# Kernel optimization log

Measured on AMD Instinct MI355X. Metric: run time of the kernel, lower is better.

## Reference

```python
import jax, jax.numpy as jnp
import numpy as np

N_HEADS = 2


def _ln(x, g, b, eps=1e-5):
    m = x.mean(-1, keepdims=True)
    v = ((x - m) ** 2).mean(-1, keepdims=True)
    return (x - m) * jax.lax.rsqrt(v + eps) * g + b


def _mha(x, in_w, in_b, out_w, out_b):
    # standard multi-head self-attention (relative/rotary branch is inert: query_pos=None)
    B, S, d = x.shape
    hd = d // N_HEADS
    qkv = x @ in_w.T + in_b
    q, k, v = jnp.split(qkv, 3, axis=-1)
    q = q.reshape(B, S, N_HEADS, hd)
    k = k.reshape(B, S, N_HEADS, hd)
    v = v.reshape(B, S, N_HEADS, hd)
    scores = jnp.einsum('bqhd,bkhd->bhqk', q, k) / jnp.sqrt(jnp.asarray(hd, x.dtype))
    attn = jax.nn.softmax(scores, axis=-1)
    o = jnp.einsum('bhqk,bkhd->bqhd', attn, v).reshape(B, S, d)
    return o @ out_w.T + out_b


def _forward(x, w1, b1, attn_in_w, attn_in_b, attn_out_w, attn_out_b, ln1_g, ln1_b,
             ffw_w1, ffw_b1, ffw_w2, ffw_b2, ln2_g, ln2_b,
             in_proj_w, conv_w, conv_b, x_proj_w, dt_proj_w, dt_proj_b, A_log, D, out_proj_w,
             w2a, b2a, w2b, b2b, w3a, b3a, w3b, b3b):
    # mlp1: (B,S,1) -> (B,S,d)
    h = x @ w1.T + b1
    # FFWRelativeSelfAttentionModule: 2 layers of post-norm MHA + FFW, take last output
    for i in range(2):
        a = _mha(h, attn_in_w[i], attn_in_b[i], attn_out_w[i], attn_out_b[i])
        h = _ln(h + a, ln1_g[i], ln1_b[i])
        f = jax.nn.relu(h @ ffw_w1[i].T + ffw_b1[i]) @ ffw_w2[i].T + ffw_b2[i]
        h = _ln(h + f, ln2_g[i], ln2_b[i])
    # Mamba block
    xz = h @ in_proj_w.T                       # (B,S,2*di)
    xm, z = jnp.split(xz, 2, axis=-1)          # (B,S,di) each
    S_len = xm.shape[1]
    dcv = conv_w.shape[1]
    xp = jnp.pad(xm, ((0, 0), (dcv - 1, 0), (0, 0)))   # causal depthwise conv1d
    xc = conv_b + sum(conv_w[:, k] * xp[:, k:k + S_len, :] for k in range(dcv))
    xc = jax.nn.silu(xc)
    xdb = xc @ x_proj_w.T                      # (B,S,dt_rank+2*N)
    dt_r = dt_proj_w.shape[1]
    N = A_log.shape[1]
    dti = xdb[..., :dt_r]
    Bm = xdb[..., dt_r:dt_r + N]
    Cm = xdb[..., dt_r + N:]
    dt = jax.nn.softplus(dti @ dt_proj_w.T + dt_proj_b)   # (B,S,di)
    A = -jnp.exp(A_log)                                    # (di,N)

    def step(hst, inp):
        dt_t, B_t, C_t, x_t = inp              # (B,di),(B,N),(B,N),(B,di)
        hst = hst * jnp.exp(dt_t[..., None] * A) + dt_t[..., None] * B_t[:, None, :] * x_t[..., None]
        y = jnp.einsum('bdn,bn->bd', hst, C_t)
        return hst, y

    h0 = jnp.zeros((xc.shape[0], A.shape[0], N), xc.dtype)
    xs = (jnp.swapaxes(dt, 0, 1), jnp.swapaxes(Bm, 0, 1),
          jnp.swapaxes(Cm, 0, 1), jnp.swapaxes(xc, 0, 1))
    _, ys = jax.lax.scan(step, h0, xs)
    y = jnp.swapaxes(ys, 0, 1) + D * xc
    y = y * jax.nn.silu(z)
    h = y @ out_proj_w.T                       # (B,S,d)
    # mlp2 (two stacked Linears, no activation) -> (B,S,1)
    o = (h @ w2a.T + b2a) @ w2b.T + b2b
    o = o.reshape(o.shape[0], -1)              # (B,9)
    # mlp3
    o = jax.nn.relu(o @ w3a.T + b3a) @ w3b.T + b3b
    return o


def setup_inputs() -> dict:
    key = jax.random.key(0)
    ks = jax.random.split(key, 16)
    d, N, dcv, di, dtr, B, S = 256, 16, 4, 512, 16, 4096, 9
    rn = lambda k, shp, s=0.02: jax.random.normal(k, shp, jnp.float32) * s
    return {
        'x': jax.random.normal(ks[0], (B, S, 1), jnp.float32),
        'w1': rn(ks[1], (d, 1), 0.5), 'b1': jnp.zeros((d,)),
        'attn_in_w': rn(ks[2], (2, 3 * d, d)), 'attn_in_b': jnp.zeros((2, 3 * d)),
        'attn_out_w': rn(ks[3], (2, d, d)), 'attn_out_b': jnp.zeros((2, d)),
        'ln1_g': jnp.ones((2, d)), 'ln1_b': jnp.zeros((2, d)),
        'ffw_w1': rn(ks[4], (2, d, d)), 'ffw_b1': jnp.zeros((2, d)),
        'ffw_w2': rn(ks[5], (2, d, d)), 'ffw_b2': jnp.zeros((2, d)),
        'ln2_g': jnp.ones((2, d)), 'ln2_b': jnp.zeros((2, d)),
        'in_proj_w': rn(ks[6], (2 * di, d)),
        'conv_w': rn(ks[7], (di, dcv), 0.2), 'conv_b': jnp.zeros((di,)),
        'x_proj_w': rn(ks[8], (dtr + 2 * N, di)),
        'dt_proj_w': rn(ks[9], (di, dtr), 0.1), 'dt_proj_b': jnp.full((di,), -4.0),
        'A_log': jnp.log(jnp.broadcast_to(jnp.arange(1, N + 1, dtype=jnp.float32), (di, N))),
        'D': jnp.ones((di,)),
        'out_proj_w': rn(ks[10], (d, di)),
        'w2a': rn(ks[11], (32, d)), 'b2a': jnp.zeros((32,)),
        'w2b': rn(ks[12], (1, 32)), 'b2b': jnp.zeros((1,)),
        'w3a': rn(ks[13], (9, 9), 0.3), 'b3a': jnp.zeros((9,)),
        'w3b': rn(ks[14], (1, 9), 0.3), 'b3b': jnp.zeros((1,)),
    }


def reference(x, w1, b1, attn_in_w, attn_in_b, attn_out_w, attn_out_b, ln1_g, ln1_b,
              ffw_w1, ffw_b1, ffw_w2, ffw_b2, ln2_g, ln2_b,
              in_proj_w, conv_w, conv_b, x_proj_w, dt_proj_w, dt_proj_b, A_log, D, out_proj_w,
              w2a, b2a, w2b, b2b, w3a, b3a, w3b, b3b):
    return _forward(x, w1, b1, attn_in_w, attn_in_b, attn_out_w, attn_out_b, ln1_g, ln1_b,
                    ffw_w1, ffw_b1, ffw_w2, ffw_b2, ln2_g, ln2_b,
                    in_proj_w, conv_w, conv_b, x_proj_w, dt_proj_w, dt_proj_b, A_log, D, out_proj_w,
                    w2a, b2a, w2b, b2b, w3a, b3a, w3b, b3b)
```

## Files before the change

kernel.cpp:

```cpp
#include <hip/hip_runtime.h>
#include <hip/hip_bf16.h>
#include <math.h>


#define BATCH 4096

typedef __attribute__((ext_vector_type(8))) short short8;
typedef __attribute__((ext_vector_type(4))) float f32x4;
typedef __attribute__((ext_vector_type(4))) unsigned short u16x4;
typedef unsigned short ushort;

#define GLD16(gp, lp) __builtin_amdgcn_global_load_lds( \
    (const __attribute__((address_space(1))) unsigned int*)(gp), \
    (__attribute__((address_space(3))) unsigned int*)(lp), 16, 0, 0)

__device__ __forceinline__ ushort f2bf(float f) {
    unsigned u = __float_as_uint(f);
    u += 0x7fffu + ((u >> 16) & 1u);
    return (ushort)(u >> 16);
}
__device__ __forceinline__ float bf2f(ushort u) {
    return __uint_as_float(((unsigned)u) << 16);
}

__global__ __launch_bounds__(256) void convw_kernel(
    const float* __restrict__ s0, const float* __restrict__ s1,
    const float* __restrict__ s2, const float* __restrict__ s3,
    const float* __restrict__ s4, const float* __restrict__ s5,
    ushort* __restrict__ dst)
{
    int i = blockIdx.x * 256 + threadIdx.x;
    float v;
    if      (i < 393216)  v = s0[i];
    else if (i < 524288)  v = s1[i - 393216];
    else if (i < 655360)  v = s2[i - 524288];
    else if (i < 786432)  v = s3[i - 655360];
    else if (i < 1048576) v = s4[i - 786432];
    else                  v = s5[i - 1048576];
    dst[i] = f2bf(v);
}

__global__ __launch_bounds__(512) void headw_kernel(
    const float* __restrict__ out_proj_w,
    const float* __restrict__ w2a,
    const float* __restrict__ b2a,
    const float* __restrict__ w2b,
    const float* __restrict__ b2b,
    float* __restrict__ wcb)
{
    __shared__ float vc[256];
    const int t = threadIdx.x;
    if (t < 256) {
        float a = 0.f;
        #pragma unroll
        for (int j = 0; j < 32; ++j) a = fmaf(w2b[j], w2a[j * 256 + t], a);
        vc[t] = a;
    }
    __syncthreads();
    float a = 0.f;
    for (int c = 0; c < 256; ++c) a = fmaf(vc[c], out_proj_w[c * 512 + t], a);
    wcb[t] = a;
    if (t == 0) {
        float bc = b2b[0];
        #pragma unroll
        for (int j = 0; j < 32; ++j) bc = fmaf(w2b[j], b2a[j], bc);
        wcb[512] = bc;
    }
}

__global__ __launch_bounds__(256) void embed_kernel(
    const float* __restrict__ x, const float* __restrict__ w1,
    const float* __restrict__ b1, float* __restrict__ h,
    ushort* __restrict__ hbf, int r0, int nr)
{
    int i = blockIdx.x * 256 + threadIdx.x;
    if (i >= nr * 256) return;
    int c  = i & 255;
    int row = i >> 8;
    float v = x[r0 + row] * w1[c] + b1[c];
    h[i] = v;
    hbf[i] = f2bf(v);
}

__global__ __launch_bounds__(256) void mgemm_kernel(
    const ushort* __restrict__ A, const ushort* __restrict__ W,
    const float* __restrict__ bias, float* __restrict__ Cf,
    ushort* __restrict__ Cb, const float* __restrict__ yin,
    int M, int N, int K, int lda, int act, int outmode)
{
    __shared__ ushort As[128 * 64];
    __shared__ ushort Bs[128 * 64];

    const int tid  = threadIdx.x;
    const int m0   = blockIdx.x * 128;
    const int n0   = blockIdx.y * 128;
    const int wid  = tid >> 6, lane = tid & 63;
    const int wr   = wid >> 1, wc = wid & 1;
    const int lrow = lane & 15, lk8 = lane >> 4, l7 = lane & 7;
    const int rw   = lane >> 3, sl8 = lane & 7;

    f32x4 acc[4][4];
    #pragma unroll
    for (int i = 0; i < 4; ++i)
        #pragma unroll
        for (int j = 0; j < 4; ++j)
            acc[i][j] = f32x4{0.f, 0.f, 0.f, 0.f};

    for (int k0 = 0; k0 < K; k0 += 64) {
        const int ka = (sl8 ^ rw) * 8;
        #pragma unroll
        for (int p = 0; p < 4; ++p) {
            const int r0 = (p * 4 + wid) * 8;
            const int r  = r0 + rw;
            GLD16(&A[(size_t)(m0 + r) * lda + k0 + ka], &As[r0 * 64]);
            GLD16(&W[(size_t)(n0 + r) * K   + k0 + ka], &Bs[r0 * 64]);
        }
        __syncthreads();

        #pragma unroll
        for (int kh = 0; kh < 2; ++kh) {
            short8 af[4], bf[4];
            #pragma unroll
            for (int i = 0; i < 4; ++i) {
                const int ra = wr * 64 + i * 16 + lrow;
                const int rb = wc * 64 + i * 16 + lrow;
                const int sl = ((kh << 2) | lk8) ^ l7;
                af[i] = *reinterpret_cast<const short8*>(&As[ra * 64 + sl * 8]);
                bf[i] = *reinterpret_cast<const short8*>(&Bs[rb * 64 + sl * 8]);
            }
            #pragma unroll
            for (int i = 0; i < 4; ++i)
                #pragma unroll
                for (int j = 0; j < 4; ++j)
                    acc[i][j] = __builtin_amdgcn_mfma_f32_16x16x32_bf16(
                        af[i], bf[j], acc[i][j], 0, 0, 0);
        }
        __syncthreads();
    }

    const int cb = n0 + wc * 64 + lrow;
    const int rb = m0 + wr * 64 + lk8 * 4;
    float bj[4];
    #pragma unroll
    for (int j = 0; j < 4; ++j) bj[j] = bias ? bias[cb + j * 16] : 0.f;

    #pragma unroll
    for (int i = 0; i < 4; ++i) {
        #pragma unroll
        for (int r = 0; r < 4; ++r) {
            const size_t mrow = (size_t)(rb + i * 16 + r) * N;
            #pragma unroll
            for (int j = 0; j < 4; ++j) {
                float v = acc[i][j][r] + bj[j];
                const size_t idx = mrow + cb + j * 16;
                if (act == 1) v = fmaxf(v, 0.f);
                if (outmode == 0) {
                    Cf[idx] = v;
                } else if (outmode == 1) {
                    Cb[idx] = f2bf(v);
                } else {
                    const float sig = 1.f / (1.f + __expf(-v));
                    Cb[idx] = f2bf(yin[idx] * (v * sig));
                }
            }
        }
    }
}

__global__ __launch_bounds__(256) void sgemm_kernel(
    const float* __restrict__ A, const float* __restrict__ W,
    const float* __restrict__ bias, float* __restrict__ C,
    int M, int N, int K, int lda, int act)
{
    __shared__ float As[16][68];
    __shared__ float Ws[16][68];
    const int tid = threadIdx.x;
    const int m0 = blockIdx.y * 64;
    const int n0 = blockIdx.x * 64;
    const int tm = tid >> 4;
    const int tn = tid & 15;
    const int lrow = tid >> 2;
    const int lk   = (tid & 3) * 4;

    float acc[4][4] = {};

    for (int k0 = 0; k0 < K; k0 += 16) {
        {
            int m = m0 + lrow;
            float4 v = make_float4(0.f, 0.f, 0.f, 0.f);
            if (m < M) v = *reinterpret_cast<const float4*>(&A[(size_t)m * lda + k0 + lk]);
            As[lk + 0][lrow] = v.x; As[lk + 1][lrow] = v.y;
            As[lk + 2][lrow] = v.z; As[lk + 3][lrow] = v.w;
            int n = n0 + lrow;
            float4 w = make_float4(0.f, 0.f, 0.f, 0.f);
            if (n < N) w = *reinterpret_cast<const float4*>(&W[(size_t)n * K + k0 + lk]);
            Ws[lk + 0][lrow] = w.x; Ws[lk + 1][lrow] = w.y;
            Ws[lk + 2][lrow] = w.z; Ws[lk + 3][lrow] = w.w;
        }
        __syncthreads();
        #pragma unroll
        for (int k = 0; k < 16; ++k) {
            float4 av = *reinterpret_cast<const float4*>(&As[k][tm * 4]);
            float4 wv = *reinterpret_cast<const float4*>(&Ws[k][tn * 4]);
            float a[4] = {av.x, av.y, av.z, av.w};
            float w[4] = {wv.x, wv.y, wv.z, wv.w};
            #pragma unroll
            for (int i = 0; i < 4; ++i)
                #pragma unroll
                for (int j = 0; j < 4; ++j)
                    acc[i][j] = fmaf(a[i], w[j], acc[i][j]);
        }
        __syncthreads();
    }

    #pragma unroll
    for (int i = 0; i < 4; ++i) {
        int m = m0 + tm * 4 + i;
        if (m >= M) continue;
        #pragma unroll
        for (int j = 0; j < 4; ++j) {
            int n = n0 + tn * 4 + j;
            if (n >= N) continue;
            float v = acc[i][j];
            if (bias) v += bias[n];
            if (act == 1) v = fmaxf(v, 0.f);
            C[(size_t)m * N + n] = v;
        }
    }
}

__global__ __launch_bounds__(128) void attn_kernel(
    const ushort* __restrict__ qkv, ushort* __restrict__ o, int nb)
{
    __shared__ float q[9][132], kk[9][132], v[9][132];
    __shared__ float sc[9][12];
    const int blk = blockIdx.x;
    if (blk >= nb * 2) return;
    const int b = blk >> 1, head = blk & 1;
    const int t = threadIdx.x;
    const size_t base = (size_t)b * 9 * 768 + (size_t)head * 128;
    #pragma unroll
    for (int s = 0; s < 9; ++s) {
        q[s][t]  = bf2f(qkv[base + s * 768 + t]);
        kk[s][t] = bf2f(qkv[base + s * 768 + 256 + t]);
        v[s][t]  = bf2f(qkv[base + s * 768 + 512 + t]);
    }
    __syncthreads();
    if (t < 81) {
        int qi = t / 9, ki = t % 9;
        float acc = 0.f;
        #pragma unroll 8
        for (int c = 0; c < 128; ++c) acc = fmaf(q[qi][c], kk[ki][c], acc);
        sc[qi][ki] = acc * 0.08838834764831845f;
    }
    __syncthreads();
    if (t < 9) {
        float mx = -1e30f;
        #pragma unroll
        for (int k2 = 0; k2 < 9; ++k2) mx = fmaxf(mx, sc[t][k2]);
        float e[9], sum = 0.f;
        #pragma unroll
        for (int k2 = 0; k2 < 9; ++k2) { e[k2] = __expf(sc[t][k2] - mx); sum += e[k2]; }
        float inv = 1.f / sum;
        #pragma unroll
        for (int k2 = 0; k2 < 9; ++k2) sc[t][k2] = e[k2] * inv;
    }
    __syncthreads();
    #pragma unroll
    for (int qi = 0; qi < 9; ++qi) {
        float acc = 0.f;
        #pragma unroll
        for (int k2 = 0; k2 < 9; ++k2) acc = fmaf(sc[qi][k2], v[k2][t], acc);
        o[(size_t)(b * 9 + qi) * 256 + head * 128 + t] = f2bf(acc);
    }
}

__global__ __launch_bounds__(256) void ln_add_kernel(
    const float* __restrict__ h, const float* __restrict__ a,
    const float* __restrict__ g, const float* __restrict__ bb,
    float* __restrict__ out, ushort* __restrict__ outbf, int nrows)
{
    const int wave = threadIdx.x >> 6;
    const int lane = threadIdx.x & 63;
    const int row = blockIdx.x * 4 + wave;
    if (row >= nrows) return;
    const float4 hv = reinterpret_cast<const float4*>(h + (size_t)row * 256)[lane];
    const float4 av = reinterpret_cast<const float4*>(a + (size_t)row * 256)[lane];
    float x0 = hv.x + av.x, x1 = hv.y + av.y, x2 = hv.z + av.z, x3 = hv.w + av.w;
    float s  = x0 + x1 + x2 + x3;
    float sq = x0 * x0 + x1 * x1 + x2 * x2 + x3 * x3;
    #pragma unroll
    for (int off = 32; off; off >>= 1) {
        s  += __shfl_down(s, off);
        sq += __shfl_down(sq, off);
    }
    s = __shfl(s, 0); sq = __shfl(sq, 0);
    const float mean = s * (1.f / 256.f);
    const float var  = sq * (1.f / 256.f) - mean * mean;
    const float inv  = rsqrtf(var + 1e-5f);
    const float4 gv = reinterpret_cast<const float4*>(g)[lane];
    const float4 bv = reinterpret_cast<const float4*>(bb)[lane];
    float4 ov;
    ov.x = (x0 - mean) * inv * gv.x + bv.x;
    ov.y = (x1 - mean) * inv * gv.y + bv.y;
    ov.z = (x2 - mean) * inv * gv.z + bv.z;
    ov.w = (x3 - mean) * inv * gv.w + bv.w;
    reinterpret_cast<float4*>(out + (size_t)row * 256)[lane] = ov;
    u16x4 bf;
    bf.x = f2bf(ov.x); bf.y = f2bf(ov.y); bf.z = f2bf(ov.z); bf.w = f2bf(ov.w);
    reinterpret_cast<u16x4*>(outbf + (size_t)row * 256)[lane] = bf;
}

__global__ __launch_bounds__(256) void conv_silu2_kernel(
    const float* __restrict__ xm, const float* __restrict__ cw,
    const float* __restrict__ cb, float* __restrict__ xc, int nb)
{
    int i = blockIdx.x * 256 + threadIdx.x;
    if (i >= nb * 512) return;
    const int c = i & 511, b = i >> 9;
    float xmv[9];
    #pragma unroll
    for (int s = 0; s < 9; ++s)
        xmv[s] = xm[(size_t)(b * 9 + s) * 512 + c];
    const float4 cwv4 = *reinterpret_cast<const float4*>(&cw[c * 4]);
    const float cwv[4] = {cwv4.x, cwv4.y, cwv4.z, cwv4.w};
    const float cbv = cb[c];
    #pragma unroll
    for (int s = 0; s < 9; ++s) {
        float acc = cbv;
        #pragma unroll
        for (int k = 0; k < 4; ++k) {
            const int sp = s + k - 3;
            if (sp >= 0) acc = fmaf(cwv[k], xmv[sp], acc);
        }
        const float sig = 1.f / (1.f + __expf(-acc));
        xc[(size_t)(b * 9 + s) * 512 + c] = acc * sig;
    }
}

__global__ __launch_bounds__(512) void scan_kernel(
    float* __restrict__ xcy, const float* __restrict__ xdb,
    const float* __restrict__ dt_w, const float* __restrict__ dt_b,
    const float* __restrict__ A_log, const float* __restrict__ Dp)
{
    __shared__ float sx[9 * 48];
    const int c = threadIdx.x;
    const int b = blockIdx.x;
    if (c < 108) {
        reinterpret_cast<float4*>(sx)[c] =
            reinterpret_cast<const float4*>(xdb + (size_t)b * 432)[c];
    }

    float xcv[9];
    #pragma unroll
    for (int s = 0; s < 9; ++s)
        xcv[s] = xcy[(size_t)(b * 9 + s) * 512 + c];

    float wdt[16], Ar[16];
    #pragma unroll
    for (int n = 0; n < 16; n += 4) {
        const float4 wv4 = *reinterpret_cast<const float4*>(&dt_w[c * 16 + n]);
        wdt[n] = wv4.x; wdt[n + 1] = wv4.y; wdt[n + 2] = wv4.z; wdt[n + 3] = wv4.w;
        const float4 av4 = *reinterpret_cast<const float4*>(&A_log[c * 16 + n]);
        Ar[n] = -__expf(av4.x); Ar[n + 1] = -__expf(av4.y);
        Ar[n + 2] = -__expf(av4.z); Ar[n + 3] = -__expf(av4.w);
    }
    const float dtb = dt_b[c];
    const float Dc  = Dp[c];
    const float a1  = Ar[0];
    bool chain = true;
    #pragma unroll
    for (int n = 1; n < 16; ++n)
        chain = chain && (fabsf(Ar[n] - (float)(n + 1) * a1) <=
                          1e-3f * (float)(n + 1) * fabsf(a1));
    __syncthreads();

    float hst[16] = {};
    for (int s = 0; s < 9; ++s) {
        const float* xb = sx + s * 48;
        float dti = dtb;
        #pragma unroll
        for (int n = 0; n < 16; ++n) dti = fmaf(xb[n], wdt[n], dti);
        const float dt = (dti > 20.f) ? dti : __logf(1.f + __expf(dti));
        const float xv = xcv[s];
        const float dtx = dt * xv;
        float acc = 0.f;
        if (chain) {
            const float e1 = __expf(dt * a1);
            float en = 1.f;
            #pragma unroll
            for (int n = 0; n < 16; ++n) {
                en *= e1;
                hst[n] = fmaf(hst[n], en, dtx * xb[16 + n]);
                acc = fmaf(hst[n], xb[32 + n], acc);
            }
        } else {
            #pragma unroll
            for (int n = 0; n < 16; ++n) {
                hst[n] = fmaf(hst[n], __expf(dt * Ar[n]), dtx * xb[16 + n]);
                acc = fmaf(hst[n], xb[32 + n], acc);
            }
        }
        xcy[(size_t)(b * 9 + s) * 512 + c] = acc + Dc * xv;
    }
}

__global__ __launch_bounds__(256) void head2_kernel(
    const ushort* __restrict__ ybf, const float* __restrict__ wcb,
    const float* __restrict__ w3a, const float* __restrict__ b3a,
    const float* __restrict__ w3b, const float* __restrict__ b3b,
    float* __restrict__ out, int b0, int nb)
{
    const int wave = threadIdx.x >> 6, lane = threadIdx.x & 63;
    const int b = blockIdx.x * 4 + wave;
    if (b >= nb) return;

    float wreg[8];
    {
        const float4 w0 = *reinterpret_cast<const float4*>(&wcb[lane * 8]);
        const float4 w1 = *reinterpret_cast<const float4*>(&wcb[lane * 8 + 4]);
        wreg[0] = w0.x; wreg[1] = w0.y; wreg[2] = w0.z; wreg[3] = w0.w;
        wreg[4] = w1.x; wreg[5] = w1.y; wreg[6] = w1.z; wreg[7] = w1.w;
    }
    const float bc = wcb[512];

    float o9[9];
    #pragma unroll
    for (int s = 0; s < 9; ++s) {
        const short8 yv = *reinterpret_cast<const short8*>(
            &ybf[(size_t)(b * 9 + s) * 512 + lane * 8]);
        float acc = 0.f;
        #pragma unroll
        for (int k = 0; k < 8; ++k)
            acc = fmaf(bf2f((ushort)yv[k]), wreg[k], acc);
        #pragma unroll
        for (int off = 32; off; off >>= 1) acc += __shfl_down(acc, off);
        o9[s] = __shfl(acc, 0) + bc;
    }
    if (lane == 0) {
        float accout = b3b[0];
        #pragma unroll
        for (int j = 0; j < 9; ++j) {
            float rj = b3a[j];
            #pragma unroll
            for (int s = 0; s < 9; ++s) rj = fmaf(o9[s], w3a[j * 9 + s], rj);
            rj = fmaxf(rj, 0.f);
            accout = fmaf(rj, w3b[j], accout);
        }
        out[b0 + b] = accout;
    }
}

extern "C" void kernel_launch(void* const* d_in, const int* in_sizes, int n_in,
                              void* d_out, int out_size, void* d_ws, size_t ws_size,
                              hipStream_t stream)
{
    const float* x          = (const float*)d_in[0];
    const float* w1         = (const float*)d_in[1];
    const float* b1         = (const float*)d_in[2];
    const float* attn_in_w  = (const float*)d_in[3];
    const float* attn_in_b  = (const float*)d_in[4];
    const float* attn_out_w = (const float*)d_in[5];
    const float* attn_out_b = (const float*)d_in[6];
    const float* ln1_g      = (const float*)d_in[7];
    const float* ln1_b      = (const float*)d_in[8];
    const float* ffw_w1     = (const float*)d_in[9];
    const float* ffw_b1     = (const float*)d_in[10];
    const float* ffw_w2     = (const float*)d_in[11];
    const float* ffw_b2     = (const float*)d_in[12];
    const float* ln2_g      = (const float*)d_in[13];
    const float* ln2_b      = (const float*)d_in[14];
    const float* in_proj_w  = (const float*)d_in[15];
    const float* conv_w     = (const float*)d_in[16];
    const float* conv_b     = (const float*)d_in[17];
    const float* x_proj_w   = (const float*)d_in[18];
    const float* dt_proj_w  = (const float*)d_in[19];
    const float* dt_proj_b  = (const float*)d_in[20];
    const float* A_log      = (const float*)d_in[21];
    const float* Dp         = (const float*)d_in[22];
    const float* out_proj_w = (const float*)d_in[23];
    const float* w2a        = (const float*)d_in[24];
    const float* b2a        = (const float*)d_in[25];
    const float* w2b        = (const float*)d_in[26];
    const float* b2b        = (const float*)d_in[27];
    const float* w3a        = (const float*)d_in[28];
    const float* b3a        = (const float*)d_in[29];
    const float* w3b        = (const float*)d_in[30];
    const float* b3b        = (const float*)d_in[31];
    float* out = (float*)d_out;

    const size_t WB_FLOATS = 589824;
    const size_t HW_FLOATS = 1024;
    const size_t PER_ROW = 1792;
    int nchunks = 1;
    while (nchunks < 32 &&
           (WB_FLOATS + HW_FLOATS +
            (size_t)(BATCH / nchunks) * 9 * PER_ROW) * sizeof(float) > ws_size)
        nchunks <<= 1;
    const int nb = BATCH / nchunks;
    const int nr = nb * 9;
    const size_t CAPR = (size_t)nr;

    ushort* WB  = (ushort*)d_ws;
    float*  wcb = (float*)d_ws + WB_FLOATS;
    float*  AR  = wcb + HW_FLOATS;

    ushort* wb_attn_in  = WB;
    ushort* wb_attn_out = WB + 393216;
    ushort* wb_ffw1     = WB + 524288;
    ushort* wb_ffw2     = WB + 655360;
    ushort* wb_inproj_x = WB + 786432;
    ushort* wb_inproj_z = WB + 917504;

    hipLaunchKernelGGL(convw_kernel, dim3(1179648 / 256), dim3(256), 0, stream,
                       attn_in_w, attn_out_w, ffw_w1, ffw_w2, in_proj_w,
                       out_proj_w, WB);
    hipLaunchKernelGGL(headw_kernel, dim3(1), dim3(512), 0, stream,
                       out_proj_w, w2a, b2a, w2b, b2b, wcb);

    auto gemm = [&](const float* A, const float* W, const float* bias, float* C,
                    int M, int N, int K, int lda, int act) {
        dim3 grid((N + 63) / 64, (M + 63) / 64);
        hipLaunchKernelGGL(sgemm_kernel, grid, dim3(256), 0, stream,
                           A, W, bias, C, M, N, K, lda, act);
    };
    auto mgemm = [&](const ushort* A, const ushort* W, const float* bias,
                     float* Cf, ushort* Cb, const float* yin,
                     int M, int N, int K, int lda, int act, int outmode) {
        dim3 grid(M / 128, N / 128);
        hipLaunchKernelGGL(mgemm_kernel, grid, dim3(256), 0, stream,
                           A, W, bias, Cf, Cb, yin, M, N, K, lda, act, outmode);
    };

    for (int ck = 0; ck < nchunks; ++ck) {
        const int b0 = ck * nb;
        const int r0 = b0 * 9;

        float*  h    = AR;
        ushort* hbf  = (ushort*)(AR + CAPR * 256);
        float*  aux  = AR + CAPR * 384;
        ushort* aobf = (ushort*)aux;
        float*  big  = AR + CAPR * 512;
        ushort* qkvb = (ushort*)big;
        float*  aa   = big;
        ushort* f1bf = (ushort*)(big + CAPR * 256);
        float*  f2   = big + CAPR * 384;
        float*  xm   = big;
        ushort* ybf  = (ushort*)(big + CAPR * 512);
        float*  xc   = AR + CAPR * 1280;
        float*  xdb  = aux;

        hipLaunchKernelGGL(embed_kernel, dim3((nr * 256 + 255) / 256), dim3(256),
                           0, stream, x, w1, b1, h, hbf, r0, nr);

        for (int i = 0; i < 2; ++i) {
            mgemm(hbf, wb_attn_in + (size_t)i * 196608, attn_in_b + i * 768,
                  nullptr, qkvb, nullptr, nr, 768, 256, 256, 0, 1);
            hipLaunchKernelGGL(attn_kernel, dim3(nb * 2), dim3(128), 0, stream,
                               qkvb, aobf, nb);
            mgemm(aobf, wb_attn_out + (size_t)i * 65536, attn_out_b + i * 256,
                  aa, nullptr, nullptr, nr, 256, 256, 256, 0, 0);
            hipLaunchKernelGGL(ln_add_kernel, dim3((nr + 3) / 4), dim3(256), 0, stream,
                               h, aa, ln1_g + i * 256, ln1_b + i * 256, h, hbf, nr);
            mgemm(hbf, wb_ffw1 + (size_t)i * 65536, ffw_b1 + i * 256,
                  nullptr, f1bf, nullptr, nr, 256, 256, 256, 1, 1);
            mgemm(f1bf, wb_ffw2 + (size_t)i * 65536, ffw_b2 + i * 256,
                  f2, nullptr, nullptr, nr, 256, 256, 256, 0, 0);
            hipLaunchKernelGGL(ln_add_kernel, dim3((nr + 3) / 4), dim3(256), 0, stream,
                               h, f2, ln2_g + i * 256, ln2_b + i * 256, h, hbf, nr);
        }

        mgemm(hbf, wb_inproj_x, nullptr, xm, nullptr, nullptr,
              nr, 512, 256, 256, 0, 0);
        hipLaunchKernelGGL(conv_silu2_kernel, dim3((nb * 512 + 255) / 256), dim3(256),
                           0, stream, xm, conv_w, conv_b, xc, nb);
        gemm(xc, x_proj_w, nullptr, xdb, nr, 48, 512, 512, 0);
        hipLaunchKernelGGL(scan_kernel, dim3(nb), dim3(512), 0, stream,
                           xc, xdb, dt_proj_w, dt_proj_b, A_log, Dp);
        mgemm(hbf, wb_inproj_z, nullptr, nullptr, ybf, xc,
              nr, 512, 256, 256, 0, 2);
        hipLaunchKernelGGL(head2_kernel, dim3((nb + 3) / 4), dim3(256), 0, stream,
                           ybf, wcb, w3a, b3a, w3b, b3b, out, b0, nb);
    }
}
```

Baseline: 673.7 us.

## Fuse output GEMMs with residual-add LayerNorm and use power-tree decay in scan

Adds a GEMM kernel covering a full 256-wide output row per block (128x256 tile, 512 threads) that adds bias and residual, reduces row statistics across waves through shared memory, and writes normalized fp32 and bf16 outputs. It replaces the attn-out and FFW2 GEMMs plus their separate ln_add kernels, removing four fp32 intermediate round trips per layer and four launches. The scan's chained decay powers are now built from squared powers instead of a serial multiply chain, which shortens the dependency chain. The fused kernel has fewer blocks and uses more shared memory, so occupancy drops. Its fp32 stores are strided rather than vectorized.

```diff
diff --git a/kernel.cpp b/kernel.cpp
--- a/kernel.cpp
+++ b/kernel.cpp
@@ -167,6 +167,126 @@
     }
 }
 
+__global__ __launch_bounds__(512) void mgemm_ln_kernel(
+    const ushort* __restrict__ A, const ushort* __restrict__ W,
+    const float* __restrict__ bias, const float* __restrict__ g,
+    const float* __restrict__ bb, float* __restrict__ h,
+    ushort* __restrict__ hbf, int M, int K, int lda)
+{
+    __shared__ ushort As[128 * 64];
+    __shared__ ushort Bs[256 * 64];
+    __shared__ float lsum[128][4];
+    __shared__ float lsq[128][4];
+    __shared__ float lmean[128], linv[128];
+
+    const int tid  = threadIdx.x;
+    const int m0   = blockIdx.x * 128;
+    const int wid  = tid >> 6, lane = tid & 63;
+    const int wr   = wid >> 2, wc = wid & 3;
+    const int lrow = lane & 15, lk8 = lane >> 4, l7 = lane & 7;
+    const int rw   = lane >> 3, sl8 = lane & 7;
+
+    f32x4 acc[4][4];
+    #pragma unroll
+    for (int i = 0; i < 4; ++i)
+        #pragma unroll
+        for (int j = 0; j < 4; ++j)
+            acc[i][j] = f32x4{0.f, 0.f, 0.f, 0.f};
+
+    for (int k0 = 0; k0 < K; k0 += 64) {
+        const int ka = (sl8 ^ rw) * 8;
+        #pragma unroll
+        for (int q = 0; q < 2; ++q) {
+            const int r0 = (wid * 2 + q) * 8;
+            GLD16(&A[(size_t)(m0 + r0 + rw) * lda + k0 + ka], &As[r0 * 64]);
+        }
+        #pragma unroll
+        for (int q = 0; q < 4; ++q) {
+            const int r0 = (wid * 4 + q) * 8;
+            GLD16(&W[(size_t)(r0 + rw) * K + k0 + ka], &Bs[r0 * 64]);
+        }
+        __syncthreads();
+
+        #pragma unroll
+        for (int kh = 0; kh < 2; ++kh) {
+            short8 af[4], bf[4];
+            #pragma unroll
+            for (int i = 0; i < 4; ++i) {
+                const int ra = wr * 64 + i * 16 + lrow;
+                const int rb = wc * 64 + i * 16 + lrow;
+                const int sl = ((kh << 2) | lk8) ^ l7;
+                af[i] = *reinterpret_cast<const short8*>(&As[ra * 64 + sl * 8]);
+                bf[i] = *reinterpret_cast<const short8*>(&Bs[rb * 64 + sl * 8]);
+            }
+            #pragma unroll
+            for (int i = 0; i < 4; ++i)
+                #pragma unroll
+                for (int j = 0; j < 4; ++j)
+                    acc[i][j] = __builtin_amdgcn_mfma_f32_16x16x32_bf16(
+                        af[i], bf[j], acc[i][j], 0, 0, 0);
+        }
+        __syncthreads();
+    }
+
+    const int cb  = wc * 64 + lrow;
+    const int lr0 = wr * 64 + lk8 * 4;
+    float bj[4];
+    #pragma unroll
+    for (int j = 0; j < 4; ++j) bj[j] = bias[cb + j * 16];
+
+    #pragma unroll
+    for (int i = 0; i < 4; ++i) {
+        #pragma unroll
+        for (int r = 0; r < 4; ++r) {
+            const int lr = lr0 + i * 16 + r;
+            const size_t grow = (size_t)(m0 + lr) * 256;
+            float s = 0.f, q = 0.f;
+            #pragma unroll
+            for (int j = 0; j < 4; ++j) {
+                float v = acc[i][j][r] + bj[j] + h[grow + cb + j * 16];
+                acc[i][j][r] = v;
+                s += v; q += v * v;
+            }
+            #pragma unroll
+            for (int mm = 1; mm < 16; mm <<= 1) {
+                s += __shfl_xor(s, mm);
+                q += __shfl_xor(q, mm);
+            }
+            if (lrow == 0) { lsum[lr][wc] = s; lsq[lr][wc] = q; }
+        }
+    }
+    __syncthreads();
+    if (tid < 128) {
+        const float s = lsum[tid][0] + lsum[tid][1] + lsum[tid][2] + lsum[tid][3];
+        const float q = lsq[tid][0] + lsq[tid][1] + lsq[tid][2] + lsq[tid][3];
+        const float mean = s * (1.f / 256.f);
+        const float var  = q * (1.f / 256.f) - mean * mean;
+        lmean[tid] = mean;
+        linv[tid]  = rsqrtf(var + 1e-5f);
+    }
+    __syncthreads();
+
+    float gv[4], bv[4];
+    #pragma unroll
+    for (int j = 0; j < 4; ++j) { gv[j] = g[cb + j * 16]; bv[j] = bb[cb + j * 16]; }
+
+    #pragma unroll
+    for (int i = 0; i < 4; ++i) {
+        #pragma unroll
+        for (int r = 0; r < 4; ++r) {
+            const int lr = lr0 + i * 16 + r;
+            const size_t grow = (size_t)(m0 + lr) * 256;
+            const float mean = lmean[lr], inv = linv[lr];
+            #pragma unroll
+            for (int j = 0; j < 4; ++j) {
+                const float v = (acc[i][j][r] - mean) * inv * gv[j] + bv[j];
+                h[grow + cb + j * 16] = v;
+                hbf[grow + cb + j * 16] = f2bf(v);
+            }
+        }
+    }
+}
+
 __global__ __launch_bounds__(256) void sgemm_kernel(
     const float* __restrict__ A, const float* __restrict__ W,
     const float* __restrict__ bias, float* __restrict__ C,
@@ -275,42 +395,6 @@
     }
 }
 
-__global__ __launch_bounds__(256) void ln_add_kernel(
-    const float* __restrict__ h, const float* __restrict__ a,
-    const float* __restrict__ g, const float* __restrict__ bb,
-    float* __restrict__ out, ushort* __restrict__ outbf, int nrows)
-{
-    const int wave = threadIdx.x >> 6;
-    const int lane = threadIdx.x & 63;
-    const int row = blockIdx.x * 4 + wave;
-    if (row >= nrows) return;
-    const float4 hv = reinterpret_cast<const float4*>(h + (size_t)row * 256)[lane];
-    const float4 av = reinterpret_cast<const float4*>(a + (size_t)row * 256)[lane];
-    float x0 = hv.x + av.x, x1 = hv.y + av.y, x2 = hv.z + av.z, x3 = hv.w + av.w;
-    float s  = x0 + x1 + x2 + x3;
-    float sq = x0 * x0 + x1 * x1 + x2 * x2 + x3 * x3;
-    #pragma unroll
-    for (int off = 32; off; off >>= 1) {
-        s  += __shfl_down(s, off);
-        sq += __shfl_down(sq, off);
-    }
-    s = __shfl(s, 0); sq = __shfl(sq, 0);
-    const float mean = s * (1.f / 256.f);
-    const float var  = sq * (1.f / 256.f) - mean * mean;
-    const float inv  = rsqrtf(var + 1e-5f);
-    const float4 gv = reinterpret_cast<const float4*>(g)[lane];
-    const float4 bv = reinterpret_cast<const float4*>(bb)[lane];
-    float4 ov;
-    ov.x = (x0 - mean) * inv * gv.x + bv.x;
-    ov.y = (x1 - mean) * inv * gv.y + bv.y;
-    ov.z = (x2 - mean) * inv * gv.z + bv.z;
-    ov.w = (x3 - mean) * inv * gv.w + bv.w;
-    reinterpret_cast<float4*>(out + (size_t)row * 256)[lane] = ov;
-    u16x4 bf;
-    bf.x = f2bf(ov.x); bf.y = f2bf(ov.y); bf.z = f2bf(ov.z); bf.w = f2bf(ov.w);
-    reinterpret_cast<u16x4*>(outbf + (size_t)row * 256)[lane] = bf;
-}
-
 __global__ __launch_bounds__(256) void conv_silu2_kernel(
     const float* __restrict__ xm, const float* __restrict__ cw,
     const float* __restrict__ cb, float* __restrict__ xc, int nb)
@@ -387,10 +471,15 @@
         float acc = 0.f;
         if (chain) {
             const float e1 = __expf(dt * a1);
-            float en = 1.f;
+            const float e2 = e1 * e1, e4 = e2 * e2, e8 = e4 * e4, e16 = e8 * e8;
             #pragma unroll
             for (int n = 0; n < 16; ++n) {
-                en *= e1;
+                const int p = n + 1;
+                float en = (p & 1) ? e1 : 1.f;
+                if (p & 2)  en = (p & 1) ? en * e2 : e2;
+                if (p & 4)  en *= e4;
+                if (p & 8)  en *= e8;
+                if (p & 16) en = e16;
                 hst[n] = fmaf(hst[n], en, dtx * xb[16 + n]);
                 acc = fmaf(hst[n], xb[32 + n], acc);
             }
@@ -542,9 +631,7 @@
         ushort* aobf = (ushort*)aux;
         float*  big  = AR + CAPR * 512;
         ushort* qkvb = (ushort*)big;
-        float*  aa   = big;
         ushort* f1bf = (ushort*)(big + CAPR * 256);
-        float*  f2   = big + CAPR * 384;
         float*  xm   = big;
         ushort* ybf  = (ushort*)(big + CAPR * 512);
         float*  xc   = AR + CAPR * 1280;
@@ -558,16 +645,16 @@
                   nullptr, qkvb, nullptr, nr, 768, 256, 256, 0, 1);
             hipLaunchKernelGGL(attn_kernel, dim3(nb * 2), dim3(128), 0, stream,
                                qkvb, aobf, nb);
-            mgemm(aobf, wb_attn_out + (size_t)i * 65536, attn_out_b + i * 256,
-                  aa, nullptr, nullptr, nr, 256, 256, 256, 0, 0);
-            hipLaunchKernelGGL(ln_add_kernel, dim3((nr + 3) / 4), dim3(256), 0, stream,
-                               h, aa, ln1_g + i * 256, ln1_b + i * 256, h, hbf, nr);
+            hipLaunchKernelGGL(mgemm_ln_kernel, dim3(nr / 128), dim3(512), 0, stream,
+                               aobf, wb_attn_out + (size_t)i * 65536,
+                               attn_out_b + i * 256, ln1_g + i * 256,
+                               ln1_b + i * 256, h, hbf, nr, 256, 256);
             mgemm(hbf, wb_ffw1 + (size_t)i * 65536, ffw_b1 + i * 256,
                   nullptr, f1bf, nullptr, nr, 256, 256, 256, 1, 1);
-            mgemm(f1bf, wb_ffw2 + (size_t)i * 65536, ffw_b2 + i * 256,
-                  f2, nullptr, nullptr, nr, 256, 256, 256, 0, 0);
-            hipLaunchKernelGGL(ln_add_kernel, dim3((nr + 3) / 4), dim3(256), 0, stream,
-                               h, f2, ln2_g + i * 256, ln2_b + i * 256, h, hbf, nr);
+            hipLaunchKernelGGL(mgemm_ln_kernel, dim3(nr / 128), dim3(512), 0, stream,
+                               f1bf, wb_ffw2 + (size_t)i * 65536,
+                               ffw_b2 + i * 256, ln2_g + i * 256,
+                               ln2_b + i * 256, h, hbf, nr, 256, 256);
         }
 
         mgemm(hbf, wb_inproj_x, nullptr, xm, nullptr, nullptr,
```

After: 688.5 us. +2.2%, slower.
